# Performance work log

Hardware: AMD Instinct MI355X
Metric: run time of the kernel (lower is better)

## Reference

```python
import jax, jax.numpy as jnp
import numpy as np


def butterfly_mult(twiddle, x):
    # twiddle: (S, M, n//2, 2, 2); x: (B, S, n); increasing_stride=True
    B, S, n = x.shape
    M = twiddle.shape[1]
    out = x
    for idx in range(M):  # loop over log2(n) stages (structural, not data dim)
        stride = 1 << idx
        g = n // (2 * stride)
        t = twiddle[:, idx].reshape(S, g, stride, 2, 2)   # (S, g, r, i, j)
        xr = out.reshape(B, S, g, 2, stride)              # (B, S, g, j, r)
        out = jnp.einsum('sgrij,bsgjr->bsgir', t, xr).reshape(B, S, n)
    return out


def butterfly_layer(x, twiddle, bias, out_size):
    # x: (..., n) with n a power of 2 (pre_process pad is a no-op)
    lead = x.shape[:-1]
    n = x.shape[-1]
    S = twiddle.shape[0]
    xb = x.reshape(-1, n)
    xb = jnp.broadcast_to(xb[:, None, :], (xb.shape[0], S, n))  # expand to nstacks
    out = butterfly_mult(twiddle, xb)
    out = out.reshape(out.shape[0], S * n)[:, :out_size] + bias[:out_size]
    return out.reshape(*lead, out_size)


def setup_inputs() -> dict:
    key = jax.random.key(0)
    ks = jax.random.split(key, 5)
    B, T, D, H = 4, 4096, 1024, 4096
    inv_sqrt2 = 1.0 / np.sqrt(2.0).astype(np.float32)
    x = jax.random.normal(ks[0], (B, T, D), jnp.float32)
    tw1 = jax.random.normal(ks[1], (4, 10, 512, 2, 2), jnp.float32) * inv_sqrt2
    b1 = jax.random.normal(ks[2], (H,), jnp.float32) * 0.02
    tw2 = jax.random.normal(ks[3], (1, 11, 1024, 2, 2), jnp.float32) * inv_sqrt2
    b2 = jax.random.normal(ks[4], (D,), jnp.float32) * 0.02
    return {"x": x, "tw1": tw1, "b1": b1, "tw2": tw2, "b2": b2}


def reference(x, tw1, b1, tw2, b2):
    # GLU: fc1 (butterfly) -> chunk -> x * sigmoid(gates) -> fc2 (butterfly)
    h = butterfly_layer(x, tw1, b1, 4096)      # (B, T, 4096)
    a, gates = jnp.split(h, 2, axis=-1)        # (B, T, 2048) each
    h = a * jax.nn.sigmoid(gates)
    return butterfly_layer(h, tw2, b2, 1024)   # (B, T, 1024)
```

## Files before the change

### kernel.cpp

```cpp
#include <hip/hip_runtime.h>
#include <cstdint>


typedef float          v4f __attribute__((ext_vector_type(4)));
typedef unsigned int   u4i __attribute__((ext_vector_type(4)));
typedef unsigned int   u2i __attribute__((ext_vector_type(2)));
typedef short          bf8 __attribute__((ext_vector_type(8)));

#define MFMA16(A, B, C) __builtin_amdgcn_mfma_f32_16x16x32_bf16(A, B, C, 0, 0, 0)

#define BAR() do {                                          \
    asm volatile("s_waitcnt lgkmcnt(0)" ::: "memory");      \
    __builtin_amdgcn_s_barrier();                           \
    asm volatile("" ::: "memory");                          \
} while (0)

__device__ __forceinline__ unsigned pk2(float a, float b) {
    unsigned ua = __float_as_uint(a) + 0x8000u;
    unsigned ub = __float_as_uint(b) + 0x8000u;
    return __builtin_amdgcn_perm(ub, ua, 0x07060302u);
}

__device__ __forceinline__ v4f ub4(u2i u) {
    v4f r;
    r.x = __uint_as_float(u.x << 16); r.y = __uint_as_float(u.x & 0xffff0000u);
    r.z = __uint_as_float(u.y << 16); r.w = __uint_as_float(u.y & 0xffff0000u);
    return r;
}

__device__ __forceinline__ float sigmf(float g) {
    return __builtin_amdgcn_rcpf(1.0f + __expf(-g));
}
__device__ __forceinline__ v4f sig4(v4f g) {
    v4f r; r.x = sigmf(g.x); r.y = sigmf(g.y); r.z = sigmf(g.z); r.w = sigmf(g.w);
    return r;
}

__device__ __forceinline__ int ab(int row, int hw) {
    return (row << 11) + (((hw) << 1) ^ ((row & 7) << 4));
}

struct MP { const float* twf; int np, rbase, rstep, j0; };
__device__ __forceinline__ MP mparams(int mid, const float* tw1, const float* tw2) {
    MP p;
    if (mid < 128)      { p.twf = tw1 + (mid >> 5) * 20480;         p.np = 512;  p.rbase = (mid & 31) * 32; p.rstep = 1;  p.j0 = 0; }
    else if (mid < 256) { p.twf = tw1 + ((mid - 128) >> 5) * 20480; p.np = 512;  p.rbase = mid & 31;        p.rstep = 32; p.j0 = 5; }
    else if (mid < 320) { p.twf = tw2; p.np = 1024; p.rbase = (mid - 256) * 32; p.rstep = 1;  p.j0 = 0; }
    else                { p.twf = tw2; p.np = 1024;
                          p.rbase = (mid & 31) + (((mid - 320) >> 5) << 10);    p.rstep = 32; p.j0 = 5; }
    return p;
}

__global__ void build_mats(const float* __restrict__ tw1,
                           const float* __restrict__ tw2,
                           unsigned short* __restrict__ wsm)
{
    __shared__ v4f            tlds[160];
    __shared__ float          slds[64];
    __shared__ unsigned short obuf[2048];
    const int t = threadIdx.x;
    const int midb = blockIdx.x * 2;

    #pragma unroll
    for (int qq = 0; qq < 3; ++qq) {
        const int q = t + qq * 64;
        if (q < 160) {
            const int ml = (q >= 80) ? 1 : 0, rem = q - ml * 80;
            const int jj = rem >> 4, pr = rem & 15;
            const MP p = mparams(midb + ml, tw1, tw2);
            const int j  = p.j0 + jj;
            const int r0 = ((pr >> jj) << (jj + 1)) | (pr & ((1 << jj) - 1));
            const int pp = p.rbase + r0 * p.rstep;
            const int tidx = ((pp >> (j + 1)) << j) | (pp & ((1 << j) - 1));
            tlds[q] = *(const v4f*)(p.twf + (size_t)(j * p.np + tidx) * 4);
        }
    }
    {
        const int ml2 = t >> 5, r = t & 31, mid = midb + ml2;
        if (mid >= 320) {
            const int l2s = mid & 31, sb = (mid - 320) >> 5;
            slds[t] = tw2[(size_t)(10 * 1024 + l2s + 32 * r) * 4 + sb];
        }
    }
    __syncthreads();

    const int ml = t >> 5, c = t & 31, mid = midb + ml;
    float v[32];
    #pragma unroll
    for (int r = 0; r < 32; ++r) v[r] = (r == c) ? 1.0f : 0.0f;

    #pragma unroll
    for (int jj = 0; jj < 5; ++jj) {
        #pragma unroll
        for (int pr = 0; pr < 16; ++pr) {
            const int r0 = ((pr >> jj) << (jj + 1)) | (pr & ((1 << jj) - 1));
            const int r1 = r0 | (1 << jj);
            const v4f T  = tlds[ml * 80 + jj * 16 + pr];
            const float a = v[r0], b = v[r1];
            v[r0] = T.x * a + T.y * b;
            v[r1] = T.z * a + T.w * b;
        }
    }
    if (mid >= 320) {
        #pragma unroll
        for (int r = 0; r < 32; ++r) v[r] *= slds[ml * 32 + r];
    }
    #pragma unroll
    for (int r = 0; r < 32; ++r) {
        const int mt   = r >> 4;
        const int lane = (r & 15) + ((c >> 3) << 4);
        obuf[((ml * 2 + mt) * 64 + lane) * 8 + (c & 7)] =
            (unsigned short)((__float_as_uint(v[r]) + 0x8000u) >> 16);
    }
    __syncthreads();
    {
        const u4i* ob = (const u4i*)obuf;
        u4i* gb = (u4i*)(wsm + (size_t)midb * 1024);
        #pragma unroll
        for (int k = 0; k < 4; ++k) gb[t * 4 + k] = ob[t * 4 + k];
    }
}

__global__ __launch_bounds__(512, 2) void glu_bfly(
    const float* __restrict__ x, const float* __restrict__ b1,
    const float* __restrict__ b2, const bf8* __restrict__ mats,
    float* __restrict__ out)
{
    extern __shared__ char lds[];
    char*           actA  = lds;
    char*           actB  = lds + 65536;
    unsigned short* b1t16 = (unsigned short*)(lds + 131072);

    const int t = threadIdx.x, w = t >> 6, l = t & 63, lr = l & 15, lk = l >> 4;
    const int row0 = blockIdx.x * 32;
    const v4f vz = {0.f, 0.f, 0.f, 0.f};

    {
        const v4f* bp = (const v4f*)(b1 + t * 8);
        const v4f a = bp[0], b = bp[1];
        const float vals[8] = {a.x, a.y, a.z, a.w, b.x, b.y, b.z, b.w};
        #pragma unroll
        for (int k = 0; k < 8; ++k) {
            const int gid = t * 8 + k, s = gid >> 10, r = gid & 1023;
            b1t16[(s << 10) + ((r & 31) << 5) + (r >> 5)] =
                (unsigned short)((__float_as_uint(vals[k]) + 0x8000u) >> 16);
        }
    }

    bf8 xf[4][2];
    #pragma unroll
    for (int gi = 0; gi < 4; ++gi)
    #pragma unroll
    for (int nh = 0; nh < 2; ++nh) {
        const float* xp = x + (size_t)(row0 + nh * 16 + lr) * 1024 + (w * 4 + gi) * 32 + lk * 8;
        const v4f a = *(const v4f*)xp, b = *(const v4f*)(xp + 4);
        u4i uu; uu.x = pk2(a.x, a.y); uu.y = pk2(a.z, a.w);
        uu.z = pk2(b.x, b.y); uu.w = pk2(b.z, b.w);
        xf[gi][nh] = __builtin_bit_cast(bf8, uu);
    }

    unsigned z0p[4][2][2][2];
    v4f fin[4][2][2];

    bf8 m1a[8];
    #pragma unroll
    for (int q = 0; q < 8; ++q)
        m1a[q] = mats[((0 * 32 + w * 4 + (q >> 1)) * 2 + (q & 1)) * 64 + l];

    #pragma unroll
    for (int h = 0; h < 2; ++h) {
        const int sa = h, sg = h + 2;

        bf8 m1b[8];
        #pragma unroll
        for (int q = 0; q < 8; ++q)
            m1b[q] = mats[((sg * 32 + w * 4 + (q >> 1)) * 2 + (q & 1)) * 64 + l];
        {
            v4f acc[4][2][2];
            __builtin_amdgcn_s_setprio(1);
            #pragma unroll
            for (int gi = 0; gi < 4; ++gi)
            #pragma unroll
            for (int nh = 0; nh < 2; ++nh) {
                acc[gi][nh][0] = MFMA16(m1a[gi * 2 + 0], xf[gi][nh], vz);
                acc[gi][nh][1] = MFMA16(m1a[gi * 2 + 1], xf[gi][nh], vz);
            }
            __builtin_amdgcn_s_setprio(0);
            #pragma unroll
            for (int nh = 0; nh < 2; ++nh)
            #pragma unroll
            for (int mt = 0; mt < 2; ++mt)
            #pragma unroll
            for (int rg = 0; rg < 4; ++rg) {
                const int m = mt * 16 + lk * 4 + rg;
                u2i pv;
                pv.x = pk2(acc[0][nh][mt][rg], acc[1][nh][mt][rg]);
                pv.y = pk2(acc[2][nh][mt][rg], acc[3][nh][mt][rg]);
                *(u2i*)(actA + ab(nh * 16 + lr, 32 * m + 4 * w)) = pv;
            }
        }
        {
            v4f acc[4][2][2];
            __builtin_amdgcn_s_setprio(1);
            #pragma unroll
            for (int gi = 0; gi < 4; ++gi)
            #pragma unroll
            for (int nh = 0; nh < 2; ++nh) {
                acc[gi][nh][0] = MFMA16(m1b[gi * 2 + 0], xf[gi][nh], vz);
                acc[gi][nh][1] = MFMA16(m1b[gi * 2 + 1], xf[gi][nh], vz);
            }
            __builtin_amdgcn_s_setprio(0);
            #pragma unroll
            for (int nh = 0; nh < 2; ++nh)
            #pragma unroll
            for (int mt = 0; mt < 2; ++mt)
            #pragma unroll
            for (int rg = 0; rg < 4; ++rg) {
                const int m = mt * 16 + lk * 4 + rg;
                u2i pv;
                pv.x = pk2(acc[0][nh][mt][rg], acc[1][nh][mt][rg]);
                pv.y = pk2(acc[2][nh][mt][rg], acc[3][nh][mt][rg]);
                *(u2i*)(actB + ab(nh * 16 + lr, 32 * m + 4 * w)) = pv;
            }
        }
        bf8 cm[4];
        cm[0] = mats[((128 + sa * 32 + w * 4 + 0) * 2 + 0) * 64 + l];
        cm[1] = mats[((128 + sa * 32 + w * 4 + 0) * 2 + 1) * 64 + l];
        cm[2] = mats[((128 + sg * 32 + w * 4 + 0) * 2 + 0) * 64 + l];
        cm[3] = mats[((128 + sg * 32 + w * 4 + 0) * 2 + 1) * 64 + l];
        BAR();

        v4f uacc[4][2][2];
        #pragma unroll
        for (int li = 0; li < 4; ++li) {
            bf8 nm[4];
            if (li < 3) {
                nm[0] = mats[((128 + sa * 32 + w * 4 + li + 1) * 2 + 0) * 64 + l];
                nm[1] = mats[((128 + sa * 32 + w * 4 + li + 1) * 2 + 1) * 64 + l];
                nm[2] = mats[((128 + sg * 32 + w * 4 + li + 1) * 2 + 0) * 64 + l];
                nm[3] = mats[((128 + sg * 32 + w * 4 + li + 1) * 2 + 1) * 64 + l];
            }
            const int lg = w * 4 + li;
            const bf8 fa0 = *(const bf8*)(actA + ab(lr,      32 * lg + 8 * lk));
            const bf8 fa1 = *(const bf8*)(actA + ab(16 + lr, 32 * lg + 8 * lk));
            const bf8 fg0 = *(const bf8*)(actB + ab(lr,      32 * lg + 8 * lk));
            const bf8 fg1 = *(const bf8*)(actB + ab(16 + lr, 32 * lg + 8 * lk));
            v4f ha[2][2], hg[2][2];
            __builtin_amdgcn_s_setprio(1);
            ha[0][0] = MFMA16(cm[0], fa0, vz); ha[0][1] = MFMA16(cm[1], fa0, vz);
            ha[1][0] = MFMA16(cm[0], fa1, vz); ha[1][1] = MFMA16(cm[1], fa1, vz);
            hg[0][0] = MFMA16(cm[2], fg0, vz); hg[0][1] = MFMA16(cm[3], fg0, vz);
            hg[1][0] = MFMA16(cm[2], fg1, vz); hg[1][1] = MFMA16(cm[3], fg1, vz);
            __builtin_amdgcn_s_setprio(0);
            const int bia = ((sa * 32 + lg) << 5) + lk * 4;
            const int big = ((sg * 32 + lg) << 5) + lk * 4;
            const v4f ba0 = ub4(*(const u2i*)&b1t16[bia]);
            const v4f ba1 = ub4(*(const u2i*)&b1t16[bia + 16]);
            const v4f bg0 = ub4(*(const u2i*)&b1t16[big]);
            const v4f bg1 = ub4(*(const u2i*)&b1t16[big + 16]);
            #pragma unroll
            for (int nh = 0; nh < 2; ++nh) {
                uacc[li][nh][0] = (ha[nh][0] + ba0) * sig4(hg[nh][0] + bg0);
                uacc[li][nh][1] = (ha[nh][1] + ba1) * sig4(hg[nh][1] + bg1);
            }
            if (li < 3) { cm[0] = nm[0]; cm[1] = nm[1]; cm[2] = nm[2]; cm[3] = nm[3]; }
        }
        bf8 m3[8];
        #pragma unroll
        for (int q = 0; q < 8; ++q)
            m3[q] = mats[((256 + 32 * h + w * 4 + (q >> 1)) * 2 + (q & 1)) * 64 + l];
        BAR();
        #pragma unroll
        for (int nh = 0; nh < 2; ++nh)
        #pragma unroll
        for (int mt = 0; mt < 2; ++mt)
        #pragma unroll
        for (int rg = 0; rg < 4; ++rg) {
            const int m = mt * 16 + lk * 4 + rg;
            u2i pv;
            pv.x = pk2(uacc[0][nh][mt][rg], uacc[1][nh][mt][rg]);
            pv.y = pk2(uacc[2][nh][mt][rg], uacc[3][nh][mt][rg]);
            *(u2i*)(actA + ab(nh * 16 + lr, 32 * m + 4 * w)) = pv;
        }
        BAR();

        {
            v4f acc[4][2][2];
            #pragma unroll
            for (int gi = 0; gi < 4; ++gi) {
                const int g = w * 4 + gi;
                #pragma unroll
                for (int nh = 0; nh < 2; ++nh) {
                    const bf8 f = *(const bf8*)(actA + ab(nh * 16 + lr, 32 * g + 8 * lk));
                    __builtin_amdgcn_s_setprio(1);
                    acc[gi][nh][0] = MFMA16(m3[gi * 2 + 0], f, vz);
                    acc[gi][nh][1] = MFMA16(m3[gi * 2 + 1], f, vz);
                    __builtin_amdgcn_s_setprio(0);
                }
            }
            bf8 m4p[4];
            m4p[0] = mats[((320 + 32 * h + w * 4 + 0) * 2 + 0) * 64 + l];
            m4p[1] = mats[((320 + 32 * h + w * 4 + 0) * 2 + 1) * 64 + l];
            m4p[2] = mats[((320 + 32 * h + w * 4 + 1) * 2 + 0) * 64 + l];
            m4p[3] = mats[((320 + 32 * h + w * 4 + 1) * 2 + 1) * 64 + l];
            #pragma unroll
            for (int nh = 0; nh < 2; ++nh)
            #pragma unroll
            for (int mt = 0; mt < 2; ++mt)
            #pragma unroll
            for (int rg = 0; rg < 4; ++rg) {
                const int m = mt * 16 + lk * 4 + rg;
                u2i pv;
                pv.x = pk2(acc[0][nh][mt][rg], acc[1][nh][mt][rg]);
                pv.y = pk2(acc[2][nh][mt][rg], acc[3][nh][mt][rg]);
                *(u2i*)(actB + ab(nh * 16 + lr, 32 * m + 4 * w)) = pv;
            }
            BAR();

            bf8 m4[4];
            m4[0] = m4p[0]; m4[1] = m4p[1]; m4[2] = m4p[2]; m4[3] = m4p[3];
            #pragma unroll
            for (int li = 0; li < 4; ++li) {
                bf8 n4[2];
                if (li < 2) {
                    n4[0] = mats[((320 + 32 * h + w * 4 + li + 2) * 2 + 0) * 64 + l];
                    n4[1] = mats[((320 + 32 * h + w * 4 + li + 2) * 2 + 1) * 64 + l];
                }
                const int lg = w * 4 + li;
                const bf8 f0 = *(const bf8*)(actB + ab(lr,      32 * lg + 8 * lk));
                const bf8 f1 = *(const bf8*)(actB + ab(16 + lr, 32 * lg + 8 * lk));
                v4f zz[2][2];
                __builtin_amdgcn_s_setprio(1);
                zz[0][0] = MFMA16(m4[(li & 1) * 2 + 0], f0, vz);
                zz[0][1] = MFMA16(m4[(li & 1) * 2 + 1], f0, vz);
                zz[1][0] = MFMA16(m4[(li & 1) * 2 + 0], f1, vz);
                zz[1][1] = MFMA16(m4[(li & 1) * 2 + 1], f1, vz);
                __builtin_amdgcn_s_setprio(0);
                if (h == 0) {
                    #pragma unroll
                    for (int nh = 0; nh < 2; ++nh)
                    #pragma unroll
                    for (int mt = 0; mt < 2; ++mt) {
                        z0p[li][nh][mt][0] = pk2(zz[nh][mt].x, zz[nh][mt].y);
                        z0p[li][nh][mt][1] = pk2(zz[nh][mt].z, zz[nh][mt].w);
                    }
                } else {
                    #pragma unroll
                    for (int nh = 0; nh < 2; ++nh)
                    #pragma unroll
                    for (int mt = 0; mt < 2; ++mt) {
                        u2i uu; uu.x = z0p[li][nh][mt][0]; uu.y = z0p[li][nh][mt][1];
                        fin[li][nh][mt] = zz[nh][mt] + ub4(uu);
                    }
                }
                if (li < 2) { m4[(li & 1) * 2 + 0] = n4[0]; m4[(li & 1) * 2 + 1] = n4[1]; }
            }
        }
        if (h == 0) {
            #pragma unroll
            for (int q = 0; q < 8; ++q)
                m1a[q] = mats[((1 * 32 + w * 4 + (q >> 1)) * 2 + (q & 1)) * 64 + l];
        }
        BAR();
    }

    #pragma unroll
    for (int nh = 0; nh < 2; ++nh) {
        #pragma unroll
        for (int mt = 0; mt < 2; ++mt)
        #pragma unroll
        for (int rg = 0; rg < 4; ++rg) {
            const int p0 = 4 * w + 32 * (mt * 16 + lk * 4 + rg);
            v4f vv;
            vv.x = fin[0][nh][mt][rg]; vv.y = fin[1][nh][mt][rg];
            vv.z = fin[2][nh][mt][rg]; vv.w = fin[3][nh][mt][rg];
            *(v4f*)(lds + (lr << 12) + ((p0 << 2) ^ ((lr & 7) << 4))) = vv;
        }
        BAR();
        {
            const int row = t >> 5, c0 = (t & 31) * 4;
            #pragma unroll
            for (int i = 0; i < 8; ++i) {
                const int col = c0 + 128 * i;
                v4f ov = *(const v4f*)(lds + (row << 12) + ((col << 2) ^ ((row & 7) << 4)));
                ov += *(const v4f*)(b2 + col);
                *(v4f*)(out + (size_t)(row0 + nh * 16 + row) * 1024 + col) = ov;
            }
        }
        BAR();
    }
}

extern "C" void kernel_launch(void* const* d_in, const int* in_sizes, int n_in,
                              void* d_out, int out_size, void* d_ws, size_t ws_size,
                              hipStream_t stream) {
    const float* x   = (const float*)d_in[0];
    const float* tw1 = (const float*)d_in[1];
    const float* b1  = (const float*)d_in[2];
    const float* tw2 = (const float*)d_in[3];
    const float* b2  = (const float*)d_in[4];

    build_mats<<<192, 64, 0, stream>>>(tw1, tw2, (unsigned short*)d_ws);

    (void)hipFuncSetAttribute((const void*)glu_bfly,
                              hipFuncAttributeMaxDynamicSharedMemorySize, 139264);
    glu_bfly<<<512, 512, 139264, stream>>>(x, b1, b2, (const bf8*)d_ws,
                                           (float*)d_out);
}
```

Measured before the change: 154.5 us.

## Drop matrix prefetch pipelining, keep h-loop rolled, merge epilogue store passes

Removes the software prefetching of butterfly matrix fragments into registers (m1a/m1b/cm/m3/m4 double buffering) and loads them just before use. The h loop is kept rolled (unroll 1) and the two first-stage passes share one loop body, which should cut register pressure and code size. It also drops the s_setprio hints and writes both 16-row halves of the output to LDS before one barrier and a single store pass. The trade is exposed global/L2 load latency for the matrix fragments in exchange for fewer VGPRs and fewer barriers.

```diff
diff --git a/kernel.cpp b/kernel.cpp
--- a/kernel.cpp
+++ b/kernel.cpp
@@ -134,6 +134,7 @@
     const int t = threadIdx.x, w = t >> 6, l = t & 63, lr = l & 15, lk = l >> 4;
     const int row0 = blockIdx.x * 32;
     const v4f vz = {0.f, 0.f, 0.f, 0.f};
+    const bf8* mp = mats + l;
 
     {
         const v4f* bp = (const v4f*)(b1 + t * 8);
@@ -162,30 +163,24 @@
     unsigned z0p[4][2][2][2];
     v4f fin[4][2][2];
 
-    bf8 m1a[8];
-    #pragma unroll
-    for (int q = 0; q < 8; ++q)
-        m1a[q] = mats[((0 * 32 + w * 4 + (q >> 1)) * 2 + (q & 1)) * 64 + l];
-
-    #pragma unroll
+    #pragma unroll 1
     for (int h = 0; h < 2; ++h) {
-        const int sa = h, sg = h + 2;
-
-        bf8 m1b[8];
-        #pragma unroll
-        for (int q = 0; q < 8; ++q)
-            m1b[q] = mats[((sg * 32 + w * 4 + (q >> 1)) * 2 + (q & 1)) * 64 + l];
-        {
+
+        #pragma unroll
+        for (int pass = 0; pass < 2; ++pass) {
+            const int s = h + pass * 2;
+            char* dst = pass ? actB : actA;
             v4f acc[4][2][2];
-            __builtin_amdgcn_s_setprio(1);
-            #pragma unroll
-            for (int gi = 0; gi < 4; ++gi)
-            #pragma unroll
-            for (int nh = 0; nh < 2; ++nh) {
-                acc[gi][nh][0] = MFMA16(m1a[gi * 2 + 0], xf[gi][nh], vz);
-                acc[gi][nh][1] = MFMA16(m1a[gi * 2 + 1], xf[gi][nh], vz);
-            }
-            __builtin_amdgcn_s_setprio(0);
+            #pragma unroll
+            for (int gi = 0; gi < 4; ++gi) {
+                const bf8 a0 = mp[((s * 32 + w * 4 + gi) * 2 + 0) * 64];
+                const bf8 a1 = mp[((s * 32 + w * 4 + gi) * 2 + 1) * 64];
+                #pragma unroll
+                for (int nh = 0; nh < 2; ++nh) {
+                    acc[gi][nh][0] = MFMA16(a0, xf[gi][nh], vz);
+                    acc[gi][nh][1] = MFMA16(a1, xf[gi][nh], vz);
+                }
+            }
             #pragma unroll
             for (int nh = 0; nh < 2; ++nh)
             #pragma unroll
@@ -196,20 +191,70 @@
                 u2i pv;
                 pv.x = pk2(acc[0][nh][mt][rg], acc[1][nh][mt][rg]);
                 pv.y = pk2(acc[2][nh][mt][rg], acc[3][nh][mt][rg]);
-                *(u2i*)(actA + ab(nh * 16 + lr, 32 * m + 4 * w)) = pv;
-            }
-        }
+                *(u2i*)(dst + ab(nh * 16 + lr, 32 * m + 4 * w)) = pv;
+            }
+        }
+        BAR();
+
+        v4f uacc[4][2][2];
+        #pragma unroll
+        for (int li = 0; li < 4; ++li) {
+            const int lg = w * 4 + li;
+            const bf8 fa0 = *(const bf8*)(actA + ab(lr,      32 * lg + 8 * lk));
+            const bf8 fa1 = *(const bf8*)(actA + ab(16 + lr, 32 * lg + 8 * lk));
+            const bf8 fg0 = *(const bf8*)(actB + ab(lr,      32 * lg + 8 * lk));
+            const bf8 fg1 = *(const bf8*)(actB + ab(16 + lr, 32 * lg + 8 * lk));
+            const int mida = 128 + h * 32 + lg, midg = 128 + (h + 2) * 32 + lg;
+            const bf8 aa0 = mp[(mida * 2 + 0) * 64];
+            const bf8 aa1 = mp[(mida * 2 + 1) * 64];
+            const bf8 ag0 = mp[(midg * 2 + 0) * 64];
+            const bf8 ag1 = mp[(midg * 2 + 1) * 64];
+            v4f ha[2][2], hg[2][2];
+            ha[0][0] = MFMA16(aa0, fa0, vz); ha[0][1] = MFMA16(aa1, fa0, vz);
+            ha[1][0] = MFMA16(aa0, fa1, vz); ha[1][1] = MFMA16(aa1, fa1, vz);
+            hg[0][0] = MFMA16(ag0, fg0, vz); hg[0][1] = MFMA16(ag1, fg0, vz);
+            hg[1][0] = MFMA16(ag0, fg1, vz); hg[1][1] = MFMA16(ag1, fg1, vz);
+            const int bia = ((h * 32 + lg) << 5) + lk * 4;
+            const int big = (((h + 2) * 32 + lg) << 5) + lk * 4;
+            const v4f ba0 = ub4(*(const u2i*)&b1t16[bia]);
+            const v4f ba1 = ub4(*(const u2i*)&b1t16[bia + 16]);
+            const v4f bg0 = ub4(*(const u2i*)&b1t16[big]);
+            const v4f bg1 = ub4(*(const u2i*)&b1t16[big + 16]);
+            #pragma unroll
+            for (int nh = 0; nh < 2; ++nh) {
+                uacc[li][nh][0] = (ha[nh][0] + ba0) * sig4(hg[nh][0] + bg0);
+                uacc[li][nh][1] = (ha[nh][1] + ba1) * sig4(hg[nh][1] + bg1);
+            }
+        }
+        BAR();
+        #pragma unroll
+        for (int nh = 0; nh < 2; ++nh)
+        #pragma unroll
+        for (int mt = 0; mt < 2; ++mt)
+        #pragma unroll
+        for (int rg = 0; rg < 4; ++rg) {
+            const int m = mt * 16 + lk * 4 + rg;
+            u2i pv;
+            pv.x = pk2(uacc[0][nh][mt][rg], uacc[1][nh][mt][rg]);
+            pv.y = pk2(uacc[2][nh][mt][rg], uacc[3][nh][mt][rg]);
+            *(u2i*)(actA + ab(nh * 16 + lr, 32 * m + 4 * w)) = pv;
+        }
+        BAR();
+
         {
             v4f acc[4][2][2];
-            __builtin_amdgcn_s_setprio(1);
-            #pragma unroll
-            for (int gi = 0; gi < 4; ++gi)
-            #pragma unroll
-            for (int nh = 0; nh < 2; ++nh) {
-                acc[gi][nh][0] = MFMA16(m1b[gi * 2 + 0], xf[gi][nh], vz);
-                acc[gi][nh][1] = MFMA16(m1b[gi * 2 + 1], xf[gi][nh], vz);
-            }
-            __builtin_amdgcn_s_setprio(0);
+            #pragma unroll
+            for (int gi = 0; gi < 4; ++gi) {
+                const int g = w * 4 + gi, mid = 256 + 32 * h + g;
+                const bf8 a0 = mp[(mid * 2 + 0) * 64];
+                const bf8 a1 = mp[(mid * 2 + 1) * 64];
+                #pragma unroll
+                for (int nh = 0; nh < 2; ++nh) {
+                    const bf8 f = *(const bf8*)(actA + ab(nh * 16 + lr, 32 * g + 8 * lk));
+                    acc[gi][nh][0] = MFMA16(a0, f, vz);
+                    acc[gi][nh][1] = MFMA16(a1, f, vz);
+                }
+            }
             #pragma unroll
             for (int nh = 0; nh < 2; ++nh)
             #pragma unroll
@@ -223,171 +268,64 @@
                 *(u2i*)(actB + ab(nh * 16 + lr, 32 * m + 4 * w)) = pv;
             }
         }
-        bf8 cm[4];
-        cm[0] = mats[((128 + sa * 32 + w * 4 + 0) * 2 + 0) * 64 + l];
-        cm[1] = mats[((128 + sa * 32 + w * 4 + 0) * 2 + 1) * 64 + l];
-        cm[2] = mats[((128 + sg * 32 + w * 4 + 0) * 2 + 0) * 64 + l];
-        cm[3] = mats[((128 + sg * 32 + w * 4 + 0) * 2 + 1) * 64 + l];
-        BAR();
-
-        v4f uacc[4][2][2];
+        BAR();
+
         #pragma unroll
         for (int li = 0; li < 4; ++li) {
-            bf8 nm[4];
-            if (li < 3) {
-                nm[0] = mats[((128 + sa * 32 + w * 4 + li + 1) * 2 + 0) * 64 + l];
-                nm[1] = mats[((128 + sa * 32 + w * 4 + li + 1) * 2 + 1) * 64 + l];
-                nm[2] = mats[((128 + sg * 32 + w * 4 + li + 1) * 2 + 0) * 64 + l];
-                nm[3] = mats[((128 + sg * 32 + w * 4 + li + 1) * 2 + 1) * 64 + l];
-            }
-            const int lg = w * 4 + li;
-            const bf8 fa0 = *(const bf8*)(actA + ab(lr,      32 * lg + 8 * lk));
-            const bf8 fa1 = *(const bf8*)(actA + ab(16 + lr, 32 * lg + 8 * lk));
-            const bf8 fg0 = *(const bf8*)(actB + ab(lr,      32 * lg + 8 * lk));
-            const bf8 fg1 = *(const bf8*)(actB + ab(16 + lr, 32 * lg + 8 * lk));
-            v4f ha[2][2], hg[2][2];
-            __builtin_amdgcn_s_setprio(1);
-            ha[0][0] = MFMA16(cm[0], fa0, vz); ha[0][1] = MFMA16(cm[1], fa0, vz);
-            ha[1][0] = MFMA16(cm[0], fa1, vz); ha[1][1] = MFMA16(cm[1], fa1, vz);
-            hg[0][0] = MFMA16(cm[2], fg0, vz); hg[0][1] = MFMA16(cm[3], fg0, vz);
-            hg[1][0] = MFMA16(cm[2], fg1, vz); hg[1][1] = MFMA16(cm[3], fg1, vz);
-            __builtin_amdgcn_s_setprio(0);
-            const int bia = ((sa * 32 + lg) << 5) + lk * 4;
-            const int big = ((sg * 32 + lg) << 5) + lk * 4;
-            const v4f ba0 = ub4(*(const u2i*)&b1t16[bia]);
-            const v4f ba1 = ub4(*(const u2i*)&b1t16[bia + 16]);
-            const v4f bg0 = ub4(*(const u2i*)&b1t16[big]);
-            const v4f bg1 = ub4(*(const u2i*)&b1t16[big + 16]);
-            #pragma unroll
-            for (int nh = 0; nh < 2; ++nh) {
-                uacc[li][nh][0] = (ha[nh][0] + ba0) * sig4(hg[nh][0] + bg0);
-                uacc[li][nh][1] = (ha[nh][1] + ba1) * sig4(hg[nh][1] + bg1);
-            }
-            if (li < 3) { cm[0] = nm[0]; cm[1] = nm[1]; cm[2] = nm[2]; cm[3] = nm[3]; }
-        }
-        bf8 m3[8];
-        #pragma unroll
-        for (int q = 0; q < 8; ++q)
-            m3[q] = mats[((256 + 32 * h + w * 4 + (q >> 1)) * 2 + (q & 1)) * 64 + l];
-        BAR();
+            const int lg = w * 4 + li, mid = 320 + 32 * h + lg;
+            const bf8 f0 = *(const bf8*)(actB + ab(lr,      32 * lg + 8 * lk));
+            const bf8 f1 = *(const bf8*)(actB + ab(16 + lr, 32 * lg + 8 * lk));
+            const bf8 a0 = mp[(mid * 2 + 0) * 64];
+            const bf8 a1 = mp[(mid * 2 + 1) * 64];
+            v4f zz[2][2];
+            zz[0][0] = MFMA16(a0, f0, vz); zz[0][1] = MFMA16(a1, f0, vz);
+            zz[1][0] = MFMA16(a0, f1, vz); zz[1][1] = MFMA16(a1, f1, vz);
+            if (h == 0) {
+                #pragma unroll
+                for (int nh = 0; nh < 2; ++nh)
+                #pragma unroll
+                for (int mt = 0; mt < 2; ++mt) {
+                    z0p[li][nh][mt][0] = pk2(zz[nh][mt].x, zz[nh][mt].y);
+                    z0p[li][nh][mt][1] = pk2(zz[nh][mt].z, zz[nh][mt].w);
+                }
+            } else {
+                #pragma unroll
+                for (int nh = 0; nh < 2; ++nh)
+                #pragma unroll
+                for (int mt = 0; mt < 2; ++mt) {
+                    u2i uu; uu.x = z0p[li][nh][mt][0]; uu.y = z0p[li][nh][mt][1];
+                    fin[li][nh][mt] = zz[nh][mt] + ub4(uu);
+                }
+            }
+        }
+        BAR();
+    }
+
+    #pragma unroll
+    for (int nh = 0; nh < 2; ++nh)
+    #pragma unroll
+    for (int mt = 0; mt < 2; ++mt)
+    #pragma unroll
+    for (int rg = 0; rg < 4; ++rg) {
+        const int p0 = 4 * w + 32 * (mt * 16 + lk * 4 + rg);
+        v4f vv;
+        vv.x = fin[0][nh][mt][rg]; vv.y = fin[1][nh][mt][rg];
+        vv.z = fin[2][nh][mt][rg]; vv.w = fin[3][nh][mt][rg];
+        *(v4f*)(lds + ((nh * 16 + lr) << 12) + ((p0 << 2) ^ ((lr & 7) << 4))) = vv;
+    }
+    BAR();
+    {
+        const int row = t >> 5, c0 = (t & 31) * 4;
         #pragma unroll
         for (int nh = 0; nh < 2; ++nh)
         #pragma unroll
-        for (int mt = 0; mt < 2; ++mt)
-        #pragma unroll
-        for (int rg = 0; rg < 4; ++rg) {
-            const int m = mt * 16 + lk * 4 + rg;
-            u2i pv;
-            pv.x = pk2(uacc[0][nh][mt][rg], uacc[1][nh][mt][rg]);
-            pv.y = pk2(uacc[2][nh][mt][rg], uacc[3][nh][mt][rg]);
-            *(u2i*)(actA + ab(nh * 16 + lr, 32 * m + 4 * w)) = pv;
-        }
-        BAR();
-
-        {
-            v4f acc[4][2][2];
-            #pragma unroll
-            for (int gi = 0; gi < 4; ++gi) {
-                const int g = w * 4 + gi;
-                #pragma unroll
-                for (int nh = 0; nh < 2; ++nh) {
-                    const bf8 f = *(const bf8*)(actA + ab(nh * 16 + lr, 32 * g + 8 * lk));
-                    __builtin_amdgcn_s_setprio(1);
-                    acc[gi][nh][0] = MFMA16(m3[gi * 2 + 0], f, vz);
-                    acc[gi][nh][1] = MFMA16(m3[gi * 2 + 1], f, vz);
-                    __builtin_amdgcn_s_setprio(0);
-                }
-            }
-            bf8 m4p[4];
-            m4p[0] = mats[((320 + 32 * h + w * 4 + 0) * 2 + 0) * 64 + l];
-            m4p[1] = mats[((320 + 32 * h + w * 4 + 0) * 2 + 1) * 64 + l];
-            m4p[2] = mats[((320 + 32 * h + w * 4 + 1) * 2 + 0) * 64 + l];
-            m4p[3] = mats[((320 + 32 * h + w * 4 + 1) * 2 + 1) * 64 + l];
-            #pragma unroll
-            for (int nh = 0; nh < 2; ++nh)
-            #pragma unroll
-            for (int mt = 0; mt < 2; ++mt)
-            #pragma unroll
-            for (int rg = 0; rg < 4; ++rg) {
-                const int m = mt * 16 + lk * 4 + rg;
-                u2i pv;
-                pv.x = pk2(acc[0][nh][mt][rg], acc[1][nh][mt][rg]);
-                pv.y = pk2(acc[2][nh][mt][rg], acc[3][nh][mt][rg]);
-                *(u2i*)(actB + ab(nh * 16 + lr, 32 * m + 4 * w)) = pv;
-            }
-            BAR();
-
-            bf8 m4[4];
-            m4[0] = m4p[0]; m4[1] = m4p[1]; m4[2] = m4p[2]; m4[3] = m4p[3];
-            #pragma unroll
-            for (int li = 0; li < 4; ++li) {
-                bf8 n4[2];
-                if (li < 2) {
-                    n4[0] = mats[((320 + 32 * h + w * 4 + li + 2) * 2 + 0) * 64 + l];
-                    n4[1] = mats[((320 + 32 * h + w * 4 + li + 2) * 2 + 1) * 64 + l];
-                }
-                const int lg = w * 4 + li;
-                const bf8 f0 = *(const bf8*)(actB + ab(lr,      32 * lg + 8 * lk));
-                const bf8 f1 = *(const bf8*)(actB + ab(16 + lr, 32 * lg + 8 * lk));
-                v4f zz[2][2];
-                __builtin_amdgcn_s_setprio(1);
-                zz[0][0] = MFMA16(m4[(li & 1) * 2 + 0], f0, vz);
-                zz[0][1] = MFMA16(m4[(li & 1) * 2 + 1], f0, vz);
-                zz[1][0] = MFMA16(m4[(li & 1) * 2 + 0], f1, vz);
-                zz[1][1] = MFMA16(m4[(li & 1) * 2 + 1], f1, vz);
-                __builtin_amdgcn_s_setprio(0);
-                if (h == 0) {
-                    #pragma unroll
-                    for (int nh = 0; nh < 2; ++nh)
-                    #pragma unroll
-                    for (int mt = 0; mt < 2; ++mt) {
-                        z0p[li][nh][mt][0] = pk2(zz[nh][mt].x, zz[nh][mt].y);
-                        z0p[li][nh][mt][1] = pk2(zz[nh][mt].z, zz[nh][mt].w);
-                    }
-                } else {
-                    #pragma unroll
-                    for (int nh = 0; nh < 2; ++nh)
-                    #pragma unroll
-                    for (int mt = 0; mt < 2; ++mt) {
-                        u2i uu; uu.x = z0p[li][nh][mt][0]; uu.y = z0p[li][nh][mt][1];
-                        fin[li][nh][mt] = zz[nh][mt] + ub4(uu);
-                    }
-                }
-                if (li < 2) { m4[(li & 1) * 2 + 0] = n4[0]; m4[(li & 1) * 2 + 1] = n4[1]; }
-            }
-        }
-        if (h == 0) {
-            #pragma unroll
-            for (int q = 0; q < 8; ++q)
-                m1a[q] = mats[((1 * 32 + w * 4 + (q >> 1)) * 2 + (q & 1)) * 64 + l];
-        }
-        BAR();
-    }
-
-    #pragma unroll
-    for (int nh = 0; nh < 2; ++nh) {
-        #pragma unroll
-        for (int mt = 0; mt < 2; ++mt)
-        #pragma unroll
-        for (int rg = 0; rg < 4; ++rg) {
-            const int p0 = 4 * w + 32 * (mt * 16 + lk * 4 + rg);
-            v4f vv;
-            vv.x = fin[0][nh][mt][rg]; vv.y = fin[1][nh][mt][rg];
-            vv.z = fin[2][nh][mt][rg]; vv.w = fin[3][nh][mt][rg];
-            *(v4f*)(lds + (lr << 12) + ((p0 << 2) ^ ((lr & 7) << 4))) = vv;
-        }
-        BAR();
-        {
-            const int row = t >> 5, c0 = (t & 31) * 4;
-            #pragma unroll
-            for (int i = 0; i < 8; ++i) {
-                const int col = c0 + 128 * i;
-                v4f ov = *(const v4f*)(lds + (row << 12) + ((col << 2) ^ ((row & 7) << 4)));
-                ov += *(const v4f*)(b2 + col);
-                *(v4f*)(out + (size_t)(row0 + nh * 16 + row) * 1024 + col) = ov;
-            }
-        }
-        BAR();
+        for (int i = 0; i < 8; ++i) {
+            const int col = c0 + 128 * i;
+            v4f ov = *(const v4f*)(lds + ((nh * 16 + row) << 12) +
+                                   ((col << 2) ^ ((row & 7) << 4)));
+            ov += *(const v4f*)(b2 + col);
+            *(v4f*)(out + (size_t)(row0 + nh * 16 + row) * 1024 + col) = ov;
+        }
     }
 }
 
```

Result: slower. 180.9 us (+17.1%).
